# Performance work log

Measured on AMD Instinct MI355X. Metric: run time of the kernel, lower is better.

## Reference

```python
import jax, jax.numpy as jnp
import numpy as np

BINS = 64

def _histc_rows(flat, bins):
    # flat: [N, L]; per-row torch.histc semantics with min=max=0 (use data min/max)
    lo = flat.min(axis=1, keepdims=True)
    hi = flat.max(axis=1, keepdims=True)
    same = hi == lo
    lo = jnp.where(same, lo - 1.0, lo)
    hi = jnp.where(same, hi + 1.0, hi)
    # bin index; value == hi maps to bins -> clipped into last bin (torch includes max)
    idx = jnp.floor((flat - lo) / (hi - lo) * bins).astype(jnp.int32)
    idx = jnp.clip(idx, 0, bins - 1)
    n = flat.shape[0]
    flat_idx = idx + (jnp.arange(n, dtype=jnp.int32)[:, None] * bins)
    hist = jnp.zeros((n * bins,), dtype=flat.dtype).at[flat_idx.ravel()].add(1.0)
    return hist.reshape(n, bins)

def reference(x, conv_w, conv_b, head_w, head_b):
    # Conv2d(1 -> C, k=3, valid), NCHW
    y = jax.lax.conv_general_dilated(
        x, conv_w, window_strides=(1, 1), padding='VALID',
        dimension_numbers=('NCHW', 'OIHW', 'NCHW'))
    y = y + conv_b[None, :, None, None]
    y = jax.nn.relu(y)
    b, c, h, w = y.shape
    hist = _histc_rows(y.reshape(b * c, h * w), BINS)  # [B*C, bins]
    feat = hist.reshape(b, c * BINS)
    return feat @ head_w.T + head_b

def setup_inputs() -> dict:
    key = jax.random.key(0)
    k1, k2, k3, k4, k5 = jax.random.split(key, 5)
    C, K, F = 64, 3, 1000
    return {
        'x': jax.random.normal(k1, (64, 1, 256, 256), dtype=jnp.float32),
        'conv_w': jax.random.normal(k2, (C, 1, K, K), dtype=jnp.float32) * 0.1,
        'conv_b': jax.random.normal(k3, (C,), dtype=jnp.float32) * 0.1,
        'head_w': jax.random.normal(k4, (F, C * BINS), dtype=jnp.float32) * 0.02,
        'head_b': jax.random.normal(k5, (F,), dtype=jnp.float32) * 0.02,
    }
```

## Files before the change

### kernel.cpp

```cpp
#include <hip/hip_runtime.h>


typedef short bf16x8 __attribute__((ext_vector_type(8)));
typedef float f32x16 __attribute__((ext_vector_type(16)));

#define TPITCH 35
#define F_OUT_ 1000
#define KDIM_ 4096

__device__ __forceinline__ unsigned f2bf(float f) {
    unsigned u = __float_as_uint(f);
    return (u + 0x7FFFu + ((u >> 16) & 1u)) >> 16;
}
__device__ __forceinline__ float bf2f(unsigned h) { return __uint_as_float(h << 16); }

__device__ __forceinline__ unsigned cvt_u32_sat(float f) {
    unsigned r;
    asm volatile("v_cvt_u32_f32 %0, %1" : "=v"(r) : "v"(f));
    return r;
}

union FragU { uint4 u; bf16x8 v; };

__global__ __launch_bounds__(512, 4) void conv_minmax_kernel(
    const float* __restrict__ x, const float* __restrict__ cw,
    const float* __restrict__ cb, float* __restrict__ featQ,
    float* __restrict__ mnbuf, float* __restrict__ mxbuf)
{
    __shared__ unsigned t32[256 * TPITCH];
    __shared__ float red[1024];

    const int tid = threadIdx.x;
    const int lane = tid & 63;
    const int w = __builtin_amdgcn_readfirstlane(tid >> 6);
    const int b = blockIdx.x;
    const int seg = blockIdx.y;
    const int mrow = lane & 31;
    const int kg = lane >> 5;
    const int r0 = seg * 32;
    const int vlim = min(32, 254 - r0);

    featQ[(seg * 64 + b) * 512 + tid] = 0.f;

    FragU bwh[2], bwl[2];
#pragma unroll
    for (int g = 0; g < 2; ++g) {
        int och = g * 32 + mrow;
        unsigned hh[8], ll[8];
#pragma unroll
        for (int j = 0; j < 8; ++j) {
            int k = kg * 8 + j, dr = k >> 2, dc = k & 3;
            float wv = (kg == 1 && j == 7) ? cb[och]
                     : ((dr < 3 && dc < 3) ? cw[och * 9 + dr * 3 + dc] : 0.f);
            unsigned h = f2bf(wv);
            hh[j] = h;
            ll[j] = f2bf(wv - bf2f(h));
        }
        bwh[g].u = make_uint4(hh[0] | (hh[1] << 16), hh[2] | (hh[3] << 16),
                              hh[4] | (hh[5] << 16), hh[6] | (hh[7] << 16));
        bwl[g].u = make_uint4(ll[0] | (ll[1] << 16), ll[2] | (ll[3] << 16),
                              ll[4] | (ll[5] << 16), ll[6] | (ll[7] << 16));
    }
    f32x16 zc;
#pragma unroll
    for (int r = 0; r < 16; ++r) zc[r] = 0.f;

    const float* xb = x + (size_t)b * 65536;
    for (int i = tid; i < TPITCH * 256; i += 512) {
        int lrow = i >> 8, col = i & 255;
        int grow = r0 + lrow;
        float v = (grow < 256) ? xb[grow * 256 + col] : 0.f;
        unsigned h = f2bf(v);
        unsigned l = f2bf(v - bf2f(h));
        t32[col * TPITCH + lrow] = (l << 16) | h;
    }
    __syncthreads();

    float mnA = 3.4e38f, mxA = -3.4e38f;
    float mnB = 3.4e38f, mxB = -3.4e38f;
    const int cbase = w * 32;
    const int cend = min(cbase + 32, 254);
    const unsigned* tb = t32 + mrow + 2 * kg;
    unsigned a0 = tb[cbase * TPITCH],       r1a = tb[cbase * TPITCH + 1];
    unsigned a1 = tb[(cbase + 1) * TPITCH], r1b = tb[(cbase + 1) * TPITCH + 1];
    unsigned a2 = tb[(cbase + 2) * TPITCH], r1c = tb[(cbase + 2) * TPITCH + 1];
#pragma unroll 2
    for (int c = cbase; c < cend; ++c) {
        int cp = min(c + 3, 255);
        unsigned a3  = tb[cp * TPITCH];
        unsigned r1d = tb[cp * TPITCH + 1];
        FragU ah, al;
        ah.u = make_uint4(__builtin_amdgcn_perm(a1, a0, 0x05040100u), a2,
                          __builtin_amdgcn_perm(r1b, r1a, 0x05040100u),
                          (r1c & 0xFFFFu) | 0x3F800000u);
        al.u = make_uint4(__builtin_amdgcn_perm(a1, a0, 0x07060302u), a2 >> 16,
                          __builtin_amdgcn_perm(r1b, r1a, 0x07060302u), r1c >> 16);
        a0 = a1; a1 = a2; a2 = a3; r1a = r1b; r1b = r1c; r1c = r1d;
        f32x16 accA = __builtin_amdgcn_mfma_f32_32x32x16_bf16(ah.v, bwh[0].v, zc, 0, 0, 0);
        f32x16 accB = __builtin_amdgcn_mfma_f32_32x32x16_bf16(ah.v, bwh[1].v, zc, 0, 0, 0);
        accA = __builtin_amdgcn_mfma_f32_32x32x16_bf16(al.v, bwh[0].v, accA, 0, 0, 0);
        accB = __builtin_amdgcn_mfma_f32_32x32x16_bf16(al.v, bwh[1].v, accB, 0, 0, 0);
        accA = __builtin_amdgcn_mfma_f32_32x32x16_bf16(ah.v, bwl[0].v, accA, 0, 0, 0);
        accB = __builtin_amdgcn_mfma_f32_32x32x16_bf16(ah.v, bwl[1].v, accB, 0, 0, 0);
        if (vlim >= 32) {
#pragma unroll
            for (int r = 0; r < 16; r += 2) {
                mnA = fminf(fminf(mnA, accA[r]), accA[r + 1]);
                mxA = fmaxf(fmaxf(mxA, accA[r]), accA[r + 1]);
                mnB = fminf(fminf(mnB, accB[r]), accB[r + 1]);
                mxB = fmaxf(fmaxf(mxB, accB[r]), accB[r + 1]);
            }
        } else {
#pragma unroll
            for (int r = 0; r < 16; ++r) {
                int crow = (r & 3) + 8 * (r >> 2) + 4 * kg;
                float vA = (crow < vlim) ? accA[r] : accA[0];
                float vB = (crow < vlim) ? accB[r] : accB[0];
                mnA = fminf(mnA, vA); mxA = fmaxf(mxA, vA);
                mnB = fminf(mnB, vB); mxB = fmaxf(mxB, vB);
            }
        }
    }

    mnA = fminf(mnA, __shfl_xor(mnA, 32, 64));
    mxA = fmaxf(mxA, __shfl_xor(mxA, 32, 64));
    mnB = fminf(mnB, __shfl_xor(mnB, 32, 64));
    mxB = fmaxf(mxB, __shfl_xor(mxB, 32, 64));
    __syncthreads();
    if (lane < 32) {
        red[w * 64 + mrow] = mnA;        red[512 + w * 64 + mrow] = mxA;
        red[w * 64 + 32 + mrow] = mnB;   red[512 + w * 64 + 32 + mrow] = mxB;
    }
    __syncthreads();
    if (tid < 64) {
        float a = red[tid], c = red[512 + tid];
#pragma unroll
        for (int i = 1; i < 8; ++i) {
            a = fminf(a, red[i * 64 + tid]);
            c = fmaxf(c, red[512 + i * 64 + tid]);
        }
        mnbuf[((b * 64 + tid) << 3) | seg] = a;
        mxbuf[((b * 64 + tid) << 3) | seg] = c;
    }
}

__global__ __launch_bounds__(512, 4) void conv_hist_kernel(
    const float* __restrict__ x, const float* __restrict__ cw,
    const float* __restrict__ cb, float* __restrict__ featQ,
    const float* __restrict__ mnbuf, const float* __restrict__ mxbuf)
{
    __shared__ unsigned t32[256 * TPITCH];
    __shared__ unsigned hist[65 * 64];

    const int tid = threadIdx.x;
    const int lane = tid & 63;
    const int w = __builtin_amdgcn_readfirstlane(tid >> 6);
    const int b = blockIdx.x;
    const int seg = blockIdx.y;
    const int mrow = lane & 31;
    const int kg = lane >> 5;
    const int r0 = seg * 32;
    const int vlim = min(32, 254 - r0);

    float scS[2], nlsS[2];
#pragma unroll
    for (int g = 0; g < 2; ++g) {
        int och = g * 32 + mrow;
        float rmn = 3.402823466e38f, rmx = -3.402823466e38f;
#pragma unroll
        for (int s = 0; s < 8; ++s) {
            rmn = fminf(rmn, mnbuf[((b * 64 + och) << 3) | s]);
            rmx = fmaxf(rmx, mxbuf[((b * 64 + och) << 3) | s]);
        }
        float lo = fmaxf(rmn, 0.f);
        float hi = fmaxf(rmx, 0.f);
        if (hi == lo) { lo -= 1.f; hi += 1.f; }
        scS[g] = 63.984f / (hi - lo);
        nlsS[g] = -lo * scS[g];
    }
    for (int i = tid; i < 65 * 64; i += 512) hist[i] = 0u;

    FragU bwh[2], bwl[2];
#pragma unroll
    for (int g = 0; g < 2; ++g) {
        int och = g * 32 + mrow;
        float sc = scS[g], nls = nlsS[g];
        unsigned hh[8], ll[8];
#pragma unroll
        for (int j = 0; j < 8; ++j) {
            int k = kg * 8 + j, dr = k >> 2, dc = k & 3;
            float wv = (kg == 1 && j == 7) ? fmaf(cb[och], sc, nls)
                     : ((dr < 3 && dc < 3) ? cw[och * 9 + dr * 3 + dc] * sc : 0.f);
            unsigned h = f2bf(wv);
            hh[j] = h;
            ll[j] = f2bf(wv - bf2f(h));
        }
        bwh[g].u = make_uint4(hh[0] | (hh[1] << 16), hh[2] | (hh[3] << 16),
                              hh[4] | (hh[5] << 16), hh[6] | (hh[7] << 16));
        bwl[g].u = make_uint4(ll[0] | (ll[1] << 16), ll[2] | (ll[3] << 16),
                              ll[4] | (ll[5] << 16), ll[6] | (ll[7] << 16));
    }
    f32x16 zc;
#pragma unroll
    for (int r = 0; r < 16; ++r) zc[r] = 0.f;

    const float* xb = x + (size_t)b * 65536;
    for (int i = tid; i < TPITCH * 256; i += 512) {
        int lrow = i >> 8, col = i & 255;
        int grow = r0 + lrow;
        float v = (grow < 256) ? xb[grow * 256 + col] : 0.f;
        unsigned h = f2bf(v);
        unsigned l = f2bf(v - bf2f(h));
        t32[col * TPITCH + lrow] = (l << 16) | h;
    }
    __syncthreads();

    const int cbase = w * 32;
    const int cend = min(cbase + 32, 254);
    unsigned* hrow = hist + mrow;
    const unsigned* tb = t32 + mrow + 2 * kg;
    unsigned a0 = tb[cbase * TPITCH],       r1a = tb[cbase * TPITCH + 1];
    unsigned a1 = tb[(cbase + 1) * TPITCH], r1b = tb[(cbase + 1) * TPITCH + 1];
    unsigned a2 = tb[(cbase + 2) * TPITCH], r1c = tb[(cbase + 2) * TPITCH + 1];
#pragma unroll 2
    for (int c = cbase; c < cend; ++c) {
        int cp = min(c + 3, 255);
        unsigned a3  = tb[cp * TPITCH];
        unsigned r1d = tb[cp * TPITCH + 1];
        FragU ah, al;
        ah.u = make_uint4(__builtin_amdgcn_perm(a1, a0, 0x05040100u), a2,
                          __builtin_amdgcn_perm(r1b, r1a, 0x05040100u),
                          (r1c & 0xFFFFu) | 0x3F800000u);
        al.u = make_uint4(__builtin_amdgcn_perm(a1, a0, 0x07060302u), a2 >> 16,
                          __builtin_amdgcn_perm(r1b, r1a, 0x07060302u), r1c >> 16);
        a0 = a1; a1 = a2; a2 = a3; r1a = r1b; r1b = r1c; r1c = r1d;
        f32x16 accA = __builtin_amdgcn_mfma_f32_32x32x16_bf16(ah.v, bwh[0].v, zc, 0, 0, 0);
        f32x16 accB = __builtin_amdgcn_mfma_f32_32x32x16_bf16(ah.v, bwh[1].v, zc, 0, 0, 0);
        accA = __builtin_amdgcn_mfma_f32_32x32x16_bf16(al.v, bwh[0].v, accA, 0, 0, 0);
        accB = __builtin_amdgcn_mfma_f32_32x32x16_bf16(al.v, bwh[1].v, accB, 0, 0, 0);
        accA = __builtin_amdgcn_mfma_f32_32x32x16_bf16(ah.v, bwl[0].v, accA, 0, 0, 0);
        accB = __builtin_amdgcn_mfma_f32_32x32x16_bf16(ah.v, bwl[1].v, accB, 0, 0, 0);
        if (vlim >= 32) {
#pragma unroll
            for (int r = 0; r < 16; ++r) {
                unsigned binA = cvt_u32_sat(accA[r]);
                unsigned binB = cvt_u32_sat(accB[r]);
                atomicAdd(&hrow[binA << 6], 1u);
                atomicAdd(&hrow[(binB << 6) + 32], 1u);
            }
        } else {
#pragma unroll
            for (int r = 0; r < 16; ++r) {
                int crow = (r & 3) + 8 * (r >> 2) + 4 * kg;
                unsigned binA = cvt_u32_sat(accA[r]);
                unsigned binB = cvt_u32_sat(accB[r]);
                if (crow >= vlim) { binA = 64u; binB = 64u; }
                atomicAdd(&hrow[binA << 6], 1u);
                atomicAdd(&hrow[(binB << 6) + 32], 1u);
            }
        }
    }
    __syncthreads();

    for (int i = tid; i < 4096; i += 512) {
        int o = i >> 6, bin = i & 63;
        float cnt = (float)hist[(bin << 6) + o];
        int k = (o << 6) | bin;
        atomicAdd(&featQ[((k >> 2) << 8) | (b << 2) | (k & 3)], cnt);
    }
}

__global__ __launch_bounds__(512) void head_kernel(
    const float* __restrict__ featQ, const float* __restrict__ hw,
    float* __restrict__ part)
{
    __shared__ float red[8][8][64];
    const int tid = threadIdx.x;
    const int m = tid & 63;
    const int kh = __builtin_amdgcn_readfirstlane(tid >> 6);
    const int n0 = blockIdx.x * 8;
    const int q = blockIdx.y;
    const int kqbase = q * 256 + kh * 32;
    const float* fb = featQ + kqbase * 256 + (m << 2);
    const float* wp[8];
#pragma unroll
    for (int c = 0; c < 8; ++c)
        wp[c] = hw + (size_t)(n0 + c) * KDIM_ + (kqbase << 2);

    float a[8] = {0.f, 0.f, 0.f, 0.f, 0.f, 0.f, 0.f, 0.f};
#pragma unroll 2
    for (int kq = 0; kq < 32; ++kq) {
        float4 f = *(const float4*)(fb + (kq << 8));
#pragma unroll
        for (int c = 0; c < 8; ++c) {
            float4 u = *(const float4*)(wp[c] + (kq << 2));
            a[c] += f.x * u.x + f.y * u.y + f.z * u.z + f.w * u.w;
        }
    }
#pragma unroll
    for (int c = 0; c < 8; ++c) red[kh][c][m] = a[c];
    __syncthreads();
    {
        int c = tid >> 6, mm = tid & 63;
        float v = 0.f;
#pragma unroll
        for (int j = 0; j < 8; ++j) v += red[j][c][mm];
        part[(size_t)q * 64000 + (n0 + c) * 64 + mm] = v;
    }
}

__global__ __launch_bounds__(256) void head_reduce_kernel(
    const float* __restrict__ part, const float* __restrict__ hb,
    float* __restrict__ out)
{
    int idx = blockIdx.x * 256 + threadIdx.x;
    int n = idx >> 6, m = idx & 63;
    float v = hb[n] + part[idx] + part[64000 + idx] +
              part[128000 + idx] + part[192000 + idx];
    out[(size_t)m * F_OUT_ + n] = v;
}

extern "C" void kernel_launch(void* const* d_in, const int* in_sizes, int n_in,
                              void* d_out, int out_size, void* d_ws, size_t ws_size,
                              hipStream_t stream) {
    const float* x      = (const float*)d_in[0];
    const float* conv_w = (const float*)d_in[1];
    const float* conv_b = (const float*)d_in[2];
    const float* head_w = (const float*)d_in[3];
    const float* head_b = (const float*)d_in[4];
    float* out   = (float*)d_out;
    float* featQ = (float*)d_ws;
    float* mnbuf = featQ + 262144;
    float* mxbuf = mnbuf + 32768;
    float* part  = mxbuf + 32768;

    dim3 g1(64, 8);
    dim3 g2(64, 8);
    conv_minmax_kernel<<<g1, 512, 0, stream>>>(x, conv_w, conv_b, featQ, mnbuf, mxbuf);
    conv_hist_kernel<<<g2, 512, 0, stream>>>(x, conv_w, conv_b, featQ, mnbuf, mxbuf);
    head_kernel<<<dim3(125, 4), 512, 0, stream>>>(featQ, head_w, part);
    head_reduce_kernel<<<250, 256, 0, stream>>>(part, head_b, out);
}
```

Baseline: 187.4 us.

## Split conv kernels across column halves to double the grid size

Both the conv/minmax and conv/histogram kernels now gain a third grid dimension that splits the 256 image columns into two 128-column halves. Each block stages only a 130-column transposed tile in LDS and each wave covers 16 columns instead of 32. The min/max partial buffers grow to 16 entries per channel, and launch bounds are raised to 6 blocks per CU. The goal is more blocks (2048 instead of 1024) and smaller LDS per block for better occupancy and load balance, at the cost of redundant halo loads, repeated weight setup, and more histogram atomics/flushes into featQ.

```diff
diff --git a/kernel.cpp b/kernel.cpp
--- a/kernel.cpp
+++ b/kernel.cpp
@@ -5,6 +5,7 @@
 typedef float f32x16 __attribute__((ext_vector_type(16)));
 
 #define TPITCH 35
+#define TCOLS 130
 #define F_OUT_ 1000
 #define KDIM_ 4096
 
@@ -22,12 +23,12 @@
 
 union FragU { uint4 u; bf16x8 v; };
 
-__global__ __launch_bounds__(512, 4) void conv_minmax_kernel(
+__global__ __launch_bounds__(512, 6) void conv_minmax_kernel(
     const float* __restrict__ x, const float* __restrict__ cw,
     const float* __restrict__ cb, float* __restrict__ featQ,
     float* __restrict__ mnbuf, float* __restrict__ mxbuf)
 {
-    __shared__ unsigned t32[256 * TPITCH];
+    __shared__ unsigned t32[TCOLS * TPITCH];
     __shared__ float red[1024];
 
     const int tid = threadIdx.x;
@@ -35,12 +36,14 @@
     const int w = __builtin_amdgcn_readfirstlane(tid >> 6);
     const int b = blockIdx.x;
     const int seg = blockIdx.y;
+    const int z = blockIdx.z;
     const int mrow = lane & 31;
     const int kg = lane >> 5;
     const int r0 = seg * 32;
+    const int c0 = z * 128;
     const int vlim = min(32, 254 - r0);
 
-    featQ[(seg * 64 + b) * 512 + tid] = 0.f;
+    if (z == 0) featQ[(seg * 64 + b) * 512 + tid] = 0.f;
 
     FragU bwh[2], bwl[2];
 #pragma unroll
@@ -66,27 +69,35 @@
     for (int r = 0; r < 16; ++r) zc[r] = 0.f;
 
     const float* xb = x + (size_t)b * 65536;
-    for (int i = tid; i < TPITCH * 256; i += 512) {
-        int lrow = i >> 8, col = i & 255;
+    for (int i = tid; i < TPITCH * 128; i += 512) {
+        int lrow = i >> 7, lcol = i & 127;
         int grow = r0 + lrow;
-        float v = (grow < 256) ? xb[grow * 256 + col] : 0.f;
+        float v = (grow < 256) ? xb[grow * 256 + c0 + lcol] : 0.f;
         unsigned h = f2bf(v);
         unsigned l = f2bf(v - bf2f(h));
-        t32[col * TPITCH + lrow] = (l << 16) | h;
+        t32[lcol * TPITCH + lrow] = (l << 16) | h;
+    }
+    if (tid < 70) {
+        int lrow = tid >> 1, lcol = 128 + (tid & 1);
+        int grow = r0 + lrow, gcol = c0 + lcol;
+        float v = (grow < 256 && gcol < 256) ? xb[grow * 256 + gcol] : 0.f;
+        unsigned h = f2bf(v);
+        unsigned l = f2bf(v - bf2f(h));
+        t32[lcol * TPITCH + lrow] = (l << 16) | h;
     }
     __syncthreads();
 
     float mnA = 3.4e38f, mxA = -3.4e38f;
     float mnB = 3.4e38f, mxB = -3.4e38f;
-    const int cbase = w * 32;
-    const int cend = min(cbase + 32, 254);
+    const int cbase = w * 16;
+    const int cend = min(cbase + 16, 254 - c0);
     const unsigned* tb = t32 + mrow + 2 * kg;
     unsigned a0 = tb[cbase * TPITCH],       r1a = tb[cbase * TPITCH + 1];
     unsigned a1 = tb[(cbase + 1) * TPITCH], r1b = tb[(cbase + 1) * TPITCH + 1];
     unsigned a2 = tb[(cbase + 2) * TPITCH], r1c = tb[(cbase + 2) * TPITCH + 1];
 #pragma unroll 2
     for (int c = cbase; c < cend; ++c) {
-        int cp = min(c + 3, 255);
+        int cp = min(c + 3, TCOLS - 1);
         unsigned a3  = tb[cp * TPITCH];
         unsigned r1d = tb[cp * TPITCH + 1];
         FragU ah, al;
@@ -139,17 +150,17 @@
             a = fminf(a, red[i * 64 + tid]);
             c = fmaxf(c, red[512 + i * 64 + tid]);
         }
-        mnbuf[((b * 64 + tid) << 3) | seg] = a;
-        mxbuf[((b * 64 + tid) << 3) | seg] = c;
-    }
-}
-
-__global__ __launch_bounds__(512, 4) void conv_hist_kernel(
+        mnbuf[((b * 64 + tid) << 4) | (seg << 1) | z] = a;
+        mxbuf[((b * 64 + tid) << 4) | (seg << 1) | z] = c;
+    }
+}
+
+__global__ __launch_bounds__(512, 6) void conv_hist_kernel(
     const float* __restrict__ x, const float* __restrict__ cw,
     const float* __restrict__ cb, float* __restrict__ featQ,
     const float* __restrict__ mnbuf, const float* __restrict__ mxbuf)
 {
-    __shared__ unsigned t32[256 * TPITCH];
+    __shared__ unsigned t32[TCOLS * TPITCH];
     __shared__ unsigned hist[65 * 64];
 
     const int tid = threadIdx.x;
@@ -157,9 +168,11 @@
     const int w = __builtin_amdgcn_readfirstlane(tid >> 6);
     const int b = blockIdx.x;
     const int seg = blockIdx.y;
+    const int z = blockIdx.z;
     const int mrow = lane & 31;
     const int kg = lane >> 5;
     const int r0 = seg * 32;
+    const int c0 = z * 128;
     const int vlim = min(32, 254 - r0);
 
     float scS[2], nlsS[2];
@@ -168,9 +181,9 @@
         int och = g * 32 + mrow;
         float rmn = 3.402823466e38f, rmx = -3.402823466e38f;
 #pragma unroll
-        for (int s = 0; s < 8; ++s) {
-            rmn = fminf(rmn, mnbuf[((b * 64 + och) << 3) | s]);
-            rmx = fmaxf(rmx, mxbuf[((b * 64 + och) << 3) | s]);
+        for (int s = 0; s < 16; ++s) {
+            rmn = fminf(rmn, mnbuf[((b * 64 + och) << 4) | s]);
+            rmx = fmaxf(rmx, mxbuf[((b * 64 + och) << 4) | s]);
         }
         float lo = fmaxf(rmn, 0.f);
         float hi = fmaxf(rmx, 0.f);
@@ -205,18 +218,26 @@
     for (int r = 0; r < 16; ++r) zc[r] = 0.f;
 
     const float* xb = x + (size_t)b * 65536;
-    for (int i = tid; i < TPITCH * 256; i += 512) {
-        int lrow = i >> 8, col = i & 255;
+    for (int i = tid; i < TPITCH * 128; i += 512) {
+        int lrow = i >> 7, lcol = i & 127;
         int grow = r0 + lrow;
-        float v = (grow < 256) ? xb[grow * 256 + col] : 0.f;
+        float v = (grow < 256) ? xb[grow * 256 + c0 + lcol] : 0.f;
         unsigned h = f2bf(v);
         unsigned l = f2bf(v - bf2f(h));
-        t32[col * TPITCH + lrow] = (l << 16) | h;
-    }
-    __syncthreads();
-
-    const int cbase = w * 32;
-    const int cend = min(cbase + 32, 254);
+        t32[lcol * TPITCH + lrow] = (l << 16) | h;
+    }
+    if (tid < 70) {
+        int lrow = tid >> 1, lcol = 128 + (tid & 1);
+        int grow = r0 + lrow, gcol = c0 + lcol;
+        float v = (grow < 256 && gcol < 256) ? xb[grow * 256 + gcol] : 0.f;
+        unsigned h = f2bf(v);
+        unsigned l = f2bf(v - bf2f(h));
+        t32[lcol * TPITCH + lrow] = (l << 16) | h;
+    }
+    __syncthreads();
+
+    const int cbase = w * 16;
+    const int cend = min(cbase + 16, 254 - c0);
     unsigned* hrow = hist + mrow;
     const unsigned* tb = t32 + mrow + 2 * kg;
     unsigned a0 = tb[cbase * TPITCH],       r1a = tb[cbase * TPITCH + 1];
@@ -224,7 +245,7 @@
     unsigned a2 = tb[(cbase + 2) * TPITCH], r1c = tb[(cbase + 2) * TPITCH + 1];
 #pragma unroll 2
     for (int c = cbase; c < cend; ++c) {
-        int cp = min(c + 3, 255);
+        int cp = min(c + 3, TCOLS - 1);
         unsigned a3  = tb[cp * TPITCH];
         unsigned r1d = tb[cp * TPITCH + 1];
         FragU ah, al;
@@ -331,11 +352,11 @@
     float* out   = (float*)d_out;
     float* featQ = (float*)d_ws;
     float* mnbuf = featQ + 262144;
-    float* mxbuf = mnbuf + 32768;
-    float* part  = mxbuf + 32768;
-
-    dim3 g1(64, 8);
-    dim3 g2(64, 8);
+    float* mxbuf = mnbuf + 65536;
+    float* part  = mxbuf + 65536;
+
+    dim3 g1(64, 8, 2);
+    dim3 g2(64, 8, 2);
     conv_minmax_kernel<<<g1, 512, 0, stream>>>(x, conv_w, conv_b, featQ, mnbuf, mxbuf);
     conv_hist_kernel<<<g2, 512, 0, stream>>>(x, conv_w, conv_b, featQ, mnbuf, mxbuf);
     head_kernel<<<dim3(125, 4), 512, 0, stream>>>(featQ, head_w, part);
```

Measured after the change: 210.2 us. 1.12x slower.
